# Performance work log

Measured on AMD Instinct MI355X. Metric: run time of the kernel, lower is better.

Reference implementation:

```python
import jax, jax.numpy as jnp
import numpy as np

B, E, H, LEVELS, MAXN = 16, 256, 256, 12, 2
N = 2 ** LEVELS - 1  # 4095 nodes, level-order perfect binary tree
NODE_VOCAB, EDGE_VOCAB = 64, 128

PARAM_SHAPES = {
    'node_emb': (NODE_VOCAB, E), 'edge_emb': (EDGE_VOCAB, E),
    'bu_Wioux': (E, 3 * H), 'bu_bioux': (3 * H,), 'bu_Wfx': (E, H), 'bu_bfx': (H,),
    'bu_Wiouh': (MAXN * H, 3 * H), 'bu_Wfh': (MAXN, MAXN * H, H),
    'bu_eWih': (E, 4 * H), 'bu_eWhh': (H, 4 * H), 'bu_ebih': (4 * H,), 'bu_ebhh': (4 * H,),
    'td_Wioux': (E, 3 * H), 'td_bioux': (3 * H,), 'td_Wfx': (E, H), 'td_bfx': (H,),
    'td_Wiouhc': (MAXN * H, 3 * H), 'td_Wiouhp': (H, 3 * H),
    'td_Wfchild': (MAXN, (MAXN + 1) * H, H), 'td_Wfparent': ((MAXN + 1) * H, H),
    'td_eWih': (E, 4 * H), 'td_eWhh': (H, 4 * H), 'td_ebih': (4 * H,), 'td_ebhh': (4 * H,),
}
FLOAT_NAMES = list(PARAM_SHAPES)

_sig = jax.nn.sigmoid

def _lstm(x, h, c, Wih, Whh, bih, bhh):
    # torch nn.LSTMCell gate order: i, f, g, o
    g = x @ Wih + h @ Whh + bih + bhh
    i, f, gg, o = jnp.split(g, 4, axis=-1)
    c2 = _sig(f) * c + _sig(i) * jnp.tanh(gg)
    return _sig(o) * jnp.tanh(c2), c2

def _forward(p, node_ids, edge_ids):
    x_all = p['node_emb'][node_ids]  # [B,N,E]
    e_all = p['edge_emb'][edge_ids]  # [B,N,E] edge to parent
    bu_h = [None] * LEVELS
    bu_he = [None] * LEVELS
    bu_ce = [None] * LEVELS
    # ---- bottom-up n-ary TreeLSTM, level by level (deepest first) ----
    for l in range(LEVELS - 1, -1, -1):
        M = 2 ** l
        s = M - 1
        x = x_all[:, s:s + M]
        if l == LEVELS - 1:  # leaves: zero-padded children (no fc terms)
            ch_h = jnp.zeros((B, M, MAXN, H), x.dtype)
            ch_c = ch_h
        else:
            ch_h = bu_he[l + 1].reshape(B, M, MAXN, H)
            ch_c = bu_ce[l + 1].reshape(B, M, MAXN, H)
        cat = ch_h.reshape(B, M, MAXN * H)  # child_cat_h
        iou = x @ p['bu_Wioux'] + p['bu_bioux'] + cat @ p['bu_Wiouh']
        i, o, u = jnp.split(iou, 3, axis=-1)
        i, o, u = _sig(i), _sig(o), jnp.tanh(u)
        fx = x @ p['bu_Wfx'] + p['bu_bfx']
        f = _sig(fx[:, :, None, :] + jnp.einsum('bmc,kch->bmkh', cat, p['bu_Wfh']))
        c = i * u + (f * ch_c).sum(axis=2)
        h = o * jnp.tanh(c)
        bu_h[l] = h
        # edge-transition LSTMCell before passing state to parent
        he, ce = _lstm(e_all[:, s:s + M], h, c, p['bu_eWih'], p['bu_eWhh'], p['bu_ebih'], p['bu_ebhh'])
        bu_he[l] = he
        bu_ce[l] = ce
    # ---- top-down n-ary TreeLSTM (root first) ----
    td_h = [None] * LEVELS
    ph = jnp.zeros((B, 1, H), x_all.dtype)
    pc = ph
    for l in range(LEVELS):
        M = 2 ** l
        s = M - 1
        x = x_all[:, s:s + M]
        if l == LEVELS - 1:
            ch_h = jnp.zeros((B, M, MAXN, H), x.dtype)
            ch_c = ch_h
        else:
            ch_h = bu_he[l + 1].reshape(B, M, MAXN, H)
            ch_c = bu_ce[l + 1].reshape(B, M, MAXN, H)
        cat = ch_h.reshape(B, M, MAXN * H)
        iou = x @ p['td_Wioux'] + p['td_bioux'] + cat @ p['td_Wiouhc'] + ph @ p['td_Wiouhp']
        i, o, u = jnp.split(iou, 3, axis=-1)
        i, o, u = _sig(i), _sig(o), jnp.tanh(u)
        fx = x @ p['td_Wfx'] + p['td_bfx']
        pcat = jnp.concatenate([ph, cat], axis=-1)  # [B,M,(MAXN+1)H]
        f_ch = _sig(fx[:, :, None, :] + jnp.einsum('bmc,kch->bmkh', pcat, p['td_Wfchild']))
        f_par = _sig(fx + pcat @ p['td_Wfparent'])
        c = i * u + (f_ch * ch_c).sum(axis=2) + f_par * pc
        h = o * jnp.tanh(c)
        td_h[l] = h
        if l < LEVELS - 1:
            M2 = 2 * M
            s2 = 2 * M - 1
            ph_r = jnp.repeat(h, 2, axis=1)
            pc_r = jnp.repeat(c, 2, axis=1)
            ph, pc = _lstm(e_all[:, s2:s2 + M2], ph_r, pc_r, p['td_eWih'], p['td_eWhh'], p['td_ebih'], p['td_ebhh'])
    return jnp.concatenate([jnp.concatenate(bu_h, 1), jnp.concatenate(td_h, 1)], axis=-1)  # [B,N,2H]


def setup_inputs() -> dict:
    key = jax.random.key(0)
    ks = jax.random.split(key, len(PARAM_SHAPES) + 2)
    inp = {}
    for k, (name, shp) in zip(ks, PARAM_SHAPES.items()):
        inp[name] = jax.random.normal(k, shp, dtype=jnp.float32) * 0.05
    inp['node_ids'] = jax.random.randint(ks[-2], (B, N), 0, NODE_VOCAB)
    inp['edge_ids'] = jax.random.randint(ks[-1], (B, N), 0, EDGE_VOCAB)
    return inp


def reference(node_emb, edge_emb, bu_Wioux, bu_bioux, bu_Wfx, bu_bfx, bu_Wiouh, bu_Wfh,
              bu_eWih, bu_eWhh, bu_ebih, bu_ebhh, td_Wioux, td_bioux, td_Wfx, td_bfx,
              td_Wiouhc, td_Wiouhp, td_Wfchild, td_Wfparent, td_eWih, td_eWhh, td_ebih, td_ebhh,
              node_ids, edge_ids):
    floats = (node_emb, edge_emb, bu_Wioux, bu_bioux, bu_Wfx, bu_bfx, bu_Wiouh, bu_Wfh,
              bu_eWih, bu_eWhh, bu_ebih, bu_ebhh, td_Wioux, td_bioux, td_Wfx, td_bfx,
              td_Wiouhc, td_Wiouhp, td_Wfchild, td_Wfparent, td_eWih, td_eWhh, td_ebih, td_ebhh)
    return _forward(dict(zip(FLOAT_NAMES, floats)), node_ids, edge_ids)
```

## Files before the change

kernel.cpp:

```cpp
#include <hip/hip_runtime.h>
#include <math.h>

#define NB 16
#define NH 256
#define NLV 12
#define NN 4095
#define OUTW 512

typedef unsigned short u16;
typedef unsigned int u32;
typedef __attribute__((ext_vector_type(4))) float f32x4;
typedef __attribute__((ext_vector_type(8))) short bf16x8;

__device__ __forceinline__ float sigf(float x){
  return __fdividef(1.0f, 1.0f + __expf(-x));
}
__device__ __forceinline__ float tanh_fast(float x){
  return 1.0f - __fdividef(2.0f, 1.0f + __expf(2.0f * x));
}

__device__ __forceinline__ u16 f2bf(float x){
  unsigned int u = __float_as_uint(x);
  return (u16)((u + 0x7fffu + ((u >> 16) & 1u)) >> 16);
}
__device__ __forceinline__ float bf2f(u16 h){
  return __uint_as_float(((unsigned int)h) << 16);
}

__device__ __forceinline__ void gload16(const void* g, void* l){
  __builtin_amdgcn_global_load_lds(
      (const __attribute__((address_space(1))) unsigned int*)g,
      (__attribute__((address_space(3))) unsigned int*)l, 16, 0, 0);
}

template<int VAR, int NG>
__global__ __launch_bounds__(256, 2) void fused_gemm(
    int R, int logM, int s,
    const int* __restrict__ ids,
    const u16* __restrict__ emb,
    const u16* __restrict__ hsrc,
    const u16* __restrict__ hsrc2,
    const u16* __restrict__ Wth, int wstride,
    const float* __restrict__ bias,
    const float* __restrict__ cce,
    const float* __restrict__ cprev,
    float* __restrict__ c_out,
    u16* __restrict__ h_out,
    float* __restrict__ out)
{
  constexpr int K0 = 256;
  constexpr int K1 = (VAR == 0) ? 512 : 256;
  constexpr int K2 = (VAR == 2 && NG == 6) ? 512 : 0;
  constexpr int KTOT = K0 + K1 + K2;
  constexpr int NSTEP = KTOT / 64;

  __shared__ u16 As[2][128][64];
  __shared__ u16 Bs[2][NG * 32][64];

  int bx = blockIdx.x;
  if ((gridDim.x & 7) == 0){
    int q = (int)gridDim.x >> 3;
    bx = (bx & 7) * q + (bx >> 3);
  }

  int tid = threadIdx.x, lane = tid & 63, w = tid >> 6;
  int wrow = w >> 1, whh = w & 1;
  int hh0 = blockIdx.y * 32;
  int M = 1 << logM;

  int lrow8 = lane >> 3;
  int gran  = lane & 7;
  int swz = (gran ^ lrow8) * 8;

  u32 off0[4]; u32 off1[4]; u32 off2[4];
  #pragma unroll
  for (int c = 0; c < 4; ++c){
    int gr = bx * 128 + c * 32 + w * 8 + lrow8;
    if (gr > R - 1) gr = R - 1;
    int b = gr >> logM, m = gr & (M - 1);
    int j = s + m;
    off0[c] = (u32)ids[b * NN + j] * 256u + (u32)swz;
    if constexpr (VAR == 0)
      off1[c] = (u32)(b * NN + 2 * j + 1) * (u32)NH + (u32)swz;
    else if constexpr (VAR == 3)
      off1[c] = (u32)(b * (M >> 1) + (m >> 1)) * (u32)NH + (u32)swz;
    else
      off1[c] = (u32)gr * (u32)NH + (u32)swz;
    if constexpr (K2 > 0)
      off2[c] = (u32)(b * NN + 2 * j + 1) * (u32)NH + (u32)swz;
    else
      off2[c] = 0;
  }
  u32 offB = (u32)(hh0 + w * 8 + lrow8) * (u32)wstride + (u32)swz;

  auto stage = [&](int buf, int kt){
    #pragma unroll
    for (int c = 0; c < 4; ++c){
      const u16* ga;
      if (kt < K0)               ga = emb   + off0[c] + kt;
      else if (kt < K0 + K1)     ga = hsrc  + off1[c] + (kt - K0);
      else                       ga = hsrc2 + off2[c] + (kt - K0 - K1);
      gload16(ga, &As[buf][c * 32 + w * 8][0]);
    }
    #pragma unroll
    for (int g = 0; g < NG; ++g)
      gload16(Wth + offB + (u32)(g * 256) * (u32)wstride + kt,
              &Bs[buf][g * 32 + w * 8][0]);
  };

  f32x4 acc[NG][4];
  #pragma unroll
  for (int g = 0; g < NG; ++g)
    #pragma unroll
    for (int i = 0; i < 4; ++i) acc[g][i] = (f32x4)0.0f;

  stage(0, 0);
  __syncthreads();

  #pragma unroll
  for (int st = 0; st < NSTEP; ++st){
    const int cur = st & 1;
    if (st + 1 < NSTEP) stage(cur ^ 1, (st + 1) * 64);

    #pragma unroll
    for (int kc = 0; kc < 2; ++kc){
      int g2 = ((kc * 4 + (lane >> 4)) ^ (lane & 7)) * 8;
      bf16x8 a[4];
      #pragma unroll
      for (int i = 0; i < 4; ++i)
        a[i] = *(const bf16x8*)&As[cur][wrow * 64 + i * 16 + (lane & 15)][g2];
      bf16x8 bf[NG];
      #pragma unroll
      for (int g = 0; g < NG; ++g)
        bf[g] = *(const bf16x8*)&Bs[cur][g * 32 + whh * 16 + (lane & 15)][g2];
      #pragma unroll
      for (int g = 0; g < NG; ++g)
        #pragma unroll
        for (int i = 0; i < 4; ++i)
          acc[g][i] = __builtin_amdgcn_mfma_f32_16x16x32_bf16(a[i], bf[g], acc[g][i], 0, 0, 0);
    }
    __syncthreads();
  }

  int hhL = hh0 + whh * 16 + (lane & 15);
  float bb[NG];
  #pragma unroll
  for (int g = 0; g < NG; ++g) bb[g] = bias[g * 256 + hhL];

  #pragma unroll
  for (int i = 0; i < 4; ++i){
    #pragma unroll
    for (int r = 0; r < 4; ++r){
      int row = bx * 128 + wrow * 64 + i * 16 + ((lane >> 4) << 2) + r;
      if (row >= R) continue;
      int b = row >> logM, m = row & (M - 1);
      int j = s + m;
      if constexpr (VAR == 0){
        float iv = sigf(acc[0][i][r] + bb[0]);
        float ov = sigf(acc[1][i][r] + bb[1]);
        float uv = tanh_fast(acc[2][i][r] + bb[2]);
        float c = iv * uv;
        float f0 = sigf(acc[3][i][r] + bb[3]);
        float f1 = sigf(acc[4 % NG][i][r] + bb[4 % NG]);
        c += f0 * cce[((size_t)(b * NN + 2 * j + 1)) * NH + hhL]
           + f1 * cce[((size_t)(b * NN + 2 * j + 2)) * NH + hhL];
        float h = ov * tanh_fast(c);
        c_out[(size_t)row * NH + hhL] = c;
        h_out[(size_t)row * NH + hhL] = f2bf(h);
        out[((size_t)(b * NN + j)) * OUTW + hhL] = h;
      } else if constexpr (VAR == 1){
        float iv = sigf(acc[0][i][r] + bb[0]);
        float fv = sigf(acc[1][i][r] + bb[1]);
        float gg = tanh_fast(acc[2][i][r] + bb[2]);
        float ov = sigf(acc[3 % NG][i][r] + bb[3 % NG]);
        float c2 = fv * cprev[(size_t)row * NH + hhL] + iv * gg;
        float h2 = ov * tanh_fast(c2);
        size_t di = ((size_t)(b * NN + j)) * NH + hhL;
        h_out[di] = f2bf(h2);
        c_out[di] = c2;
      } else if constexpr (VAR == 2){
        float iv = sigf(acc[0][i][r] + bb[0]);
        float ov = sigf(acc[1][i][r] + bb[1]);
        float uv = tanh_fast(acc[2][i][r] + bb[2]);
        float fp = sigf(acc[3 % NG][i][r] + bb[3 % NG]);
        float c = iv * uv + fp * cprev[(size_t)row * NH + hhL];
        if constexpr (NG == 6){
          float f0 = sigf(acc[4 % NG][i][r] + bb[4 % NG]);
          float f1 = sigf(acc[5 % NG][i][r] + bb[5 % NG]);
          c += f0 * cce[((size_t)(b * NN + 2 * j + 1)) * NH + hhL]
             + f1 * cce[((size_t)(b * NN + 2 * j + 2)) * NH + hhL];
        }
        float h = ov * tanh_fast(c);
        c_out[(size_t)row * NH + hhL] = c;
        h_out[(size_t)row * NH + hhL] = f2bf(h);
        out[((size_t)(b * NN + j)) * OUTW + NH + hhL] = h;
      } else {
        float iv = sigf(acc[0][i][r] + bb[0]);
        float fv = sigf(acc[1][i][r] + bb[1]);
        float gg = tanh_fast(acc[2][i][r] + bb[2]);
        float ov = sigf(acc[3 % NG][i][r] + bb[3 % NG]);
        int par = b * (M >> 1) + (m >> 1);
        float c2 = fv * cprev[(size_t)par * NH + hhL] + iv * gg;
        float h2 = ov * tanh_fast(c2);
        h_out[(size_t)row * NH + hhL] = f2bf(h2);
        c_out[(size_t)row * NH + hhL] = c2;
      }
    }
  }
}

__global__ void build_lut(int nids, int ncols, int stride, int koff,
                          const u16* __restrict__ tab,
                          const u16* __restrict__ Wt, int wstride,
                          const float* __restrict__ bias,
                          float* __restrict__ lut)
{
  int t = blockIdx.x * 256 + threadIdx.x;
  if (t >= nids * ncols) return;
  int id = t / ncols, n = t % ncols;
  const u16* e  = tab + id * 256;
  const u16* wv = Wt + (size_t)n * wstride + koff;
  float z = bias ? bias[n] : 0.0f;
  for (int k = 0; k < 256; k += 8){
    #pragma unroll
    for (int q = 0; q < 8; ++q)
      z += bf2f(e[k + q]) * bf2f(wv[k + q]);
  }
  int hh = n & 255, g = n >> 8;
  lut[((size_t)id * 256 + hh) * stride + g] = z;
}

__global__ void build_leaf(const float* __restrict__ lut64,
                           float* __restrict__ c64, float* __restrict__ h64f,
                           u16* __restrict__ h64b)
{
  int t = blockIdx.x * 256 + threadIdx.x;
  const float* lp = lut64 + (size_t)t * 3;
  float iv = sigf(lp[0]), ov = sigf(lp[1]), uv = tanh_fast(lp[2]);
  float c = iv * uv;
  float h = ov * tanh_fast(c);
  c64[t] = c; h64f[t] = h; h64b[t] = f2bf(h);
}

__global__ void leaf_gather(const int* __restrict__ node_ids,
                            const float* __restrict__ h64f,
                            float* __restrict__ out)
{
  int t = blockIdx.x * 256 + threadIdx.x;
  int gr = t >> 6, q4 = (t & 63) << 2;
  int b = gr >> 11, m = gr & 2047;
  int j = 2047 + m;
  int id = node_ids[b * NN + j];
  float4 hv = *(const float4*)(h64f + id * 256 + q4);
  *(float4*)(out + ((size_t)(b * NN + j)) * OUTW + q4) = hv;
}

__global__ void leaf_edge(const int* __restrict__ node_ids,
                          const int* __restrict__ edge_ids,
                          const float* __restrict__ lutE,
                          const float* __restrict__ lutH,
                          const float* __restrict__ c64,
                          u16* __restrict__ he_b, float* __restrict__ ce_all)
{
  int gr = blockIdx.x;
  int hh = threadIdx.x;
  int b = gr >> 11, m = gr & 2047;
  int j = 2047 + m;
  int nid = node_ids[b * NN + j];
  int eid = edge_ids[b * NN + j];
  float4 ge = *(const float4*)(lutE + ((size_t)eid * 256 + hh) * 4);
  float4 gh = *(const float4*)(lutH + ((size_t)nid * 256 + hh) * 4);
  float iv = sigf(ge.x + gh.x);
  float fv = sigf(ge.y + gh.y);
  float gg = tanh_fast(ge.z + gh.z);
  float ov = sigf(ge.w + gh.w);
  float cp = c64[nid * 256 + hh];
  float c2 = fv * cp + iv * gg;
  float h2 = ov * tanh_fast(c2);
  size_t di = ((size_t)(b * NN + j)) * NH + hh;
  he_b[di] = f2bf(h2);
  ce_all[di] = c2;
}


__global__ void pack_bu_node_t(const float* __restrict__ Wioux, const float* __restrict__ Wiouh,
                               const float* __restrict__ Wfx, const float* __restrict__ Wfh,
                               const float* __restrict__ bioux, const float* __restrict__ bfx,
                               u16* __restrict__ Wth, float* __restrict__ bd)
{
  int tid = blockIdx.x*256 + threadIdx.x;
  if (tid < 768*1280){
    int n = tid / 768, k = tid % 768;
    float v;
    if (n < 768){
      v = (k < 256) ? Wioux[k*768 + n] : Wiouh[(k-256)*768 + n];
    } else {
      int kidx = (n < 1024) ? 0 : 1;
      int nn = n - 768 - kidx*256;
      v = (k < 256) ? Wfx[k*256 + nn] : Wfh[((size_t)kidx*512 + (k-256))*256 + nn];
    }
    Wth[tid] = f2bf(v);
  }
  if (tid < 1280) bd[tid] = (tid < 768) ? bioux[tid] : bfx[(tid-768) & 255];
}

__global__ void pack_edge_t(const float* __restrict__ Wih, const float* __restrict__ Whh,
                            const float* __restrict__ bih, const float* __restrict__ bhh,
                            u16* __restrict__ Wth, float* __restrict__ bd)
{
  int tid = blockIdx.x*256 + threadIdx.x;
  if (tid < 512*1024){
    int n = tid / 512, k = tid % 512;
    float v = (k < 256) ? Wih[k*1024 + n] : Whh[(k-256)*1024 + n];
    Wth[tid] = f2bf(v);
  }
  if (tid < 1024) bd[tid] = bih[tid] + bhh[tid];
}

__global__ void pack_td_node_t(const float* __restrict__ Wioux, const float* __restrict__ Wiouhc,
                               const float* __restrict__ Wiouhp, const float* __restrict__ Wfx,
                               const float* __restrict__ Wfchild, const float* __restrict__ Wfparent,
                               const float* __restrict__ bioux, const float* __restrict__ bfx,
                               u16* __restrict__ Wth, float* __restrict__ bd)
{
  int tid = blockIdx.x*256 + threadIdx.x;
  if (tid < 1024*1536){
    int n = tid / 1024, k = tid % 1024;
    float v;
    if (n < 768){
      v = (k < 256) ? Wioux[k*768 + n]
        : (k < 512) ? Wiouhp[(k-256)*768 + n]
                    : Wiouhc[(k-512)*768 + n];
    } else if (n < 1024){
      int nn = n - 768;
      v = (k < 256) ? Wfx[k*256 + nn] : Wfparent[(size_t)(k-256)*256 + nn];
    } else {
      int kidx = (n < 1280) ? 0 : 1;
      int nn = n - 1024 - kidx*256;
      v = (k < 256) ? Wfx[k*256 + nn]
                    : Wfchild[((size_t)kidx*768 + (k-256))*256 + nn];
    }
    Wth[tid] = f2bf(v);
  }
  if (tid < 1536) bd[tid] = (tid < 768) ? bioux[tid] : bfx[(tid-768) & 255];
}

__global__ void pack_emb(const float* __restrict__ ne, const float* __restrict__ ee,
                         u16* __restrict__ neb, u16* __restrict__ eeb,
                         u16* __restrict__ ph_b, float* __restrict__ pc)
{
  int tid = blockIdx.x*256 + threadIdx.x;
  if (tid < 64*256)  neb[tid] = f2bf(ne[tid]);
  if (tid < 128*256) eeb[tid] = f2bf(ee[tid]);
  if (tid < NB*NH){ ph_b[tid] = 0; pc[tid] = 0.0f; }
}

extern "C" void kernel_launch(void* const* d_in, const int* in_sizes, int n_in,
                              void* d_out, int out_size, void* d_ws, size_t ws_size,
                              hipStream_t stream)
{
  const float* node_emb  = (const float*)d_in[0];
  const float* edge_emb  = (const float*)d_in[1];
  const float* bu_Wioux  = (const float*)d_in[2];
  const float* bu_bioux  = (const float*)d_in[3];
  const float* bu_Wfx    = (const float*)d_in[4];
  const float* bu_bfx    = (const float*)d_in[5];
  const float* bu_Wiouh  = (const float*)d_in[6];
  const float* bu_Wfh    = (const float*)d_in[7];
  const float* bu_eWih   = (const float*)d_in[8];
  const float* bu_eWhh   = (const float*)d_in[9];
  const float* bu_ebih   = (const float*)d_in[10];
  const float* bu_ebhh   = (const float*)d_in[11];
  const float* td_Wioux  = (const float*)d_in[12];
  const float* td_bioux  = (const float*)d_in[13];
  const float* td_Wfx    = (const float*)d_in[14];
  const float* td_bfx    = (const float*)d_in[15];
  const float* td_Wiouhc = (const float*)d_in[16];
  const float* td_Wiouhp = (const float*)d_in[17];
  const float* td_Wfchild= (const float*)d_in[18];
  const float* td_Wfparent=(const float*)d_in[19];
  const float* td_eWih   = (const float*)d_in[20];
  const float* td_eWhh   = (const float*)d_in[21];
  const float* td_ebih   = (const float*)d_in[22];
  const float* td_ebhh   = (const float*)d_in[23];
  const int* node_ids    = (const int*)d_in[24];
  const int* edge_ids    = (const int*)d_in[25];
  float* out = (float*)d_out;

  float* fw = (float*)d_ws;
  size_t fo = 0;
  float* bbun = fw + fo; fo += 1280;
  float* bbue = fw + fo; fo += 1024;
  float* btdn = fw + fo; fo += 1536;
  float* btde = fw + fo; fo += 1024;
  float* lut64 = fw + fo; fo += (size_t)64*256*3;
  float* c64  = fw + fo; fo += (size_t)64*256;
  float* h64f = fw + fo; fo += (size_t)64*256;
  float* lutE = fw + fo; fo += (size_t)128*256*4;
  float* lutH = fw + fo; fo += (size_t)64*256*4;
  float* ce_all = fw + fo; fo += (size_t)NB*NN*NH;
  float* c_lvl  = fw + fo; fo += (size_t)NB*2048*NH;
  float* pc     = fw + fo; fo += (size_t)NB*2048*NH;

  u16* uw = (u16*)(fw + fo);
  size_t uo = 0;
  u16* Wbunh = uw + uo; uo += (size_t)768*1280;
  u16* Wbueh = uw + uo; uo += (size_t)512*1024;
  u16* Wtdnh = uw + uo; uo += (size_t)1024*1536;
  u16* Wtdeh = uw + uo; uo += (size_t)512*1024;
  u16* neb = uw + uo; uo += (size_t)64*256;
  u16* eeb = uw + uo; uo += (size_t)128*256;
  u16* h64b = uw + uo; uo += (size_t)64*256;
  u16* he_b = uw + uo; uo += (size_t)NB*NN*NH;
  u16* hl_b = uw + uo; uo += (size_t)NB*2048*NH;
  u16* ph_b = uw + uo; uo += (size_t)NB*2048*NH;

  pack_bu_node_t<<<(768*1280+255)/256, 256, 0, stream>>>(bu_Wioux, bu_Wiouh, bu_Wfx, bu_Wfh,
      bu_bioux, bu_bfx, Wbunh, bbun);
  pack_edge_t<<<(512*1024+255)/256, 256, 0, stream>>>(bu_eWih, bu_eWhh, bu_ebih, bu_ebhh,
      Wbueh, bbue);
  pack_td_node_t<<<(1024*1536+255)/256, 256, 0, stream>>>(td_Wioux, td_Wiouhc, td_Wiouhp, td_Wfx,
      td_Wfchild, td_Wfparent, td_bioux, td_bfx, Wtdnh, btdn);
  pack_edge_t<<<(512*1024+255)/256, 256, 0, stream>>>(td_eWih, td_eWhh, td_ebih, td_ebhh,
      Wtdeh, btde);
  pack_emb<<<(128*256+255)/256, 256, 0, stream>>>(node_emb, edge_emb, neb, eeb, ph_b, pc);

  build_lut<<<(64*768+255)/256, 256, 0, stream>>>(64, 768, 3, 0, neb, Wbunh, 768, bbun, lut64);
  build_leaf<<<64, 256, 0, stream>>>(lut64, c64, h64f, h64b);
  build_lut<<<(128*1024+255)/256, 256, 0, stream>>>(128, 1024, 4, 0,   eeb,  Wbueh, 512, bbue,  lutE);
  build_lut<<<(64*1024+255)/256, 256, 0, stream>>>(64,  1024, 4, 256, h64b, Wbueh, 512, nullptr, lutH);

  {
    int R = NB * 2048;
    leaf_gather<<<(R * 64) / 256, 256, 0, stream>>>(node_ids, h64f, out);
    leaf_edge<<<R, 256, 0, stream>>>(node_ids, edge_ids, lutE, lutH, c64, he_b, ce_all);
  }
  for (int l = NLV-2; l >= 0; --l){
    int M = 1<<l, s = M-1, R = NB*M;
    dim3 grid((R + 127) / 128, NH / 32);
    fused_gemm<0,5><<<grid, 256, 0, stream>>>(R, l, s, node_ids,
        neb, he_b, neb, Wbunh, 768, bbun,
        ce_all, nullptr, c_lvl, hl_b, out);
    if (l > 0){
      fused_gemm<1,4><<<grid, 256, 0, stream>>>(R, l, s, edge_ids,
          eeb, hl_b, neb, Wbueh, 512, bbue,
          nullptr, c_lvl, ce_all, he_b, nullptr);
    }
  }

  for (int l = 0; l < NLV; ++l){
    int M = 1<<l, s = M-1, R = NB*M;
    bool leaf = (l == NLV-1);
    dim3 grid((R + 127) / 128, NH / 32);
    if (!leaf){
      fused_gemm<2,6><<<grid, 256, 0, stream>>>(R, l, s, node_ids,
          neb, ph_b, he_b, Wtdnh, 1024, btdn,
          ce_all, pc, c_lvl, hl_b, out);
      int M2 = 2*M, s2 = 2*M-1, R2 = NB*M2;
      dim3 grid2((R2 + 127) / 128, NH / 32);
      fused_gemm<3,4><<<grid2, 256, 0, stream>>>(R2, l+1, s2, edge_ids,
          eeb, hl_b, neb, Wtdeh, 512, btde,
          nullptr, c_lvl, pc, ph_b, nullptr);
    } else {
      fused_gemm<2,4><<<grid, 256, 0, stream>>>(R, l, s, node_ids,
          neb, ph_b, neb, Wtdnh, 1024, btdn,
          nullptr, pc, c_lvl, hl_b, out);
    }
  }
}
```

Measured before the change: 1.138 ms.

## Replace embedding GEMM K-slice with per-id precomputed gate lookup tables

Because node and edge embeddings come from small vocabularies, the x@W plus bias contribution is precomputed per vocab id into LUTs (stride 8 floats per hidden unit). Every fused GEMM then drops its first 256-wide K slice and adds the LUT value in the epilogue instead. This removes a quarter to a third of the MFMA and staging work per level, at the cost of extra LUT build kernels and scattered per-row LUT loads in the epilogue. The leaf edge kernel is adapted to the new stride-8 LUT layout.

```diff
diff --git a/kernel.cpp b/kernel.cpp
--- a/kernel.cpp
+++ b/kernel.cpp
@@ -37,21 +37,19 @@
 __global__ __launch_bounds__(256, 2) void fused_gemm(
     int R, int logM, int s,
     const int* __restrict__ ids,
-    const u16* __restrict__ emb,
+    const float* __restrict__ lutG,
     const u16* __restrict__ hsrc,
     const u16* __restrict__ hsrc2,
     const u16* __restrict__ Wth, int wstride,
-    const float* __restrict__ bias,
     const float* __restrict__ cce,
     const float* __restrict__ cprev,
     float* __restrict__ c_out,
     u16* __restrict__ h_out,
     float* __restrict__ out)
 {
-  constexpr int K0 = 256;
   constexpr int K1 = (VAR == 0) ? 512 : 256;
   constexpr int K2 = (VAR == 2 && NG == 6) ? 512 : 0;
-  constexpr int KTOT = K0 + K1 + K2;
+  constexpr int KTOT = K1 + K2;
   constexpr int NSTEP = KTOT / 64;
 
   __shared__ u16 As[2][128][64];
@@ -72,14 +70,13 @@
   int gran  = lane & 7;
   int swz = (gran ^ lrow8) * 8;
 
-  u32 off0[4]; u32 off1[4]; u32 off2[4];
+  u32 off1[4]; u32 off2[4];
   #pragma unroll
   for (int c = 0; c < 4; ++c){
     int gr = bx * 128 + c * 32 + w * 8 + lrow8;
     if (gr > R - 1) gr = R - 1;
     int b = gr >> logM, m = gr & (M - 1);
     int j = s + m;
-    off0[c] = (u32)ids[b * NN + j] * 256u + (u32)swz;
     if constexpr (VAR == 0)
       off1[c] = (u32)(b * NN + 2 * j + 1) * (u32)NH + (u32)swz;
     else if constexpr (VAR == 3)
@@ -91,15 +88,14 @@
     else
       off2[c] = 0;
   }
-  u32 offB = (u32)(hh0 + w * 8 + lrow8) * (u32)wstride + (u32)swz;
+  u32 offB = (u32)(hh0 + w * 8 + lrow8) * (u32)wstride + (u32)swz + 256u;
 
   auto stage = [&](int buf, int kt){
     #pragma unroll
     for (int c = 0; c < 4; ++c){
       const u16* ga;
-      if (kt < K0)               ga = emb   + off0[c] + kt;
-      else if (kt < K0 + K1)     ga = hsrc  + off1[c] + (kt - K0);
-      else                       ga = hsrc2 + off2[c] + (kt - K0 - K1);
+      if (K2 > 0 && kt >= K1) ga = hsrc2 + off2[c] + (kt - K1);
+      else                    ga = hsrc  + off1[c] + kt;
       gload16(ga, &As[buf][c * 32 + w * 8][0]);
     }
     #pragma unroll
@@ -143,9 +139,6 @@
   }
 
   int hhL = hh0 + whh * 16 + (lane & 15);
-  float bb[NG];
-  #pragma unroll
-  for (int g = 0; g < NG; ++g) bb[g] = bias[g * 256 + hhL];
 
   #pragma unroll
   for (int i = 0; i < 4; ++i){
@@ -155,13 +148,14 @@
       if (row >= R) continue;
       int b = row >> logM, m = row & (M - 1);
       int j = s + m;
+      const float* lp = lutG + ((size_t)ids[b * NN + j] * 256 + hhL) * 8;
       if constexpr (VAR == 0){
-        float iv = sigf(acc[0][i][r] + bb[0]);
-        float ov = sigf(acc[1][i][r] + bb[1]);
-        float uv = tanh_fast(acc[2][i][r] + bb[2]);
+        float iv = sigf(acc[0][i][r] + lp[0]);
+        float ov = sigf(acc[1][i][r] + lp[1]);
+        float uv = tanh_fast(acc[2][i][r] + lp[2]);
         float c = iv * uv;
-        float f0 = sigf(acc[3][i][r] + bb[3]);
-        float f1 = sigf(acc[4 % NG][i][r] + bb[4 % NG]);
+        float f0 = sigf(acc[3][i][r] + lp[3]);
+        float f1 = sigf(acc[4 % NG][i][r] + lp[4]);
         c += f0 * cce[((size_t)(b * NN + 2 * j + 1)) * NH + hhL]
            + f1 * cce[((size_t)(b * NN + 2 * j + 2)) * NH + hhL];
         float h = ov * tanh_fast(c);
@@ -169,24 +163,24 @@
         h_out[(size_t)row * NH + hhL] = f2bf(h);
         out[((size_t)(b * NN + j)) * OUTW + hhL] = h;
       } else if constexpr (VAR == 1){
-        float iv = sigf(acc[0][i][r] + bb[0]);
-        float fv = sigf(acc[1][i][r] + bb[1]);
-        float gg = tanh_fast(acc[2][i][r] + bb[2]);
-        float ov = sigf(acc[3 % NG][i][r] + bb[3 % NG]);
+        float iv = sigf(acc[0][i][r] + lp[0]);
+        float fv = sigf(acc[1][i][r] + lp[1]);
+        float gg = tanh_fast(acc[2][i][r] + lp[2]);
+        float ov = sigf(acc[3 % NG][i][r] + lp[3]);
         float c2 = fv * cprev[(size_t)row * NH + hhL] + iv * gg;
         float h2 = ov * tanh_fast(c2);
         size_t di = ((size_t)(b * NN + j)) * NH + hhL;
         h_out[di] = f2bf(h2);
         c_out[di] = c2;
       } else if constexpr (VAR == 2){
-        float iv = sigf(acc[0][i][r] + bb[0]);
-        float ov = sigf(acc[1][i][r] + bb[1]);
-        float uv = tanh_fast(acc[2][i][r] + bb[2]);
-        float fp = sigf(acc[3 % NG][i][r] + bb[3 % NG]);
+        float iv = sigf(acc[0][i][r] + lp[0]);
+        float ov = sigf(acc[1][i][r] + lp[1]);
+        float uv = tanh_fast(acc[2][i][r] + lp[2]);
+        float fp = sigf(acc[3 % NG][i][r] + lp[3]);
         float c = iv * uv + fp * cprev[(size_t)row * NH + hhL];
         if constexpr (NG == 6){
-          float f0 = sigf(acc[4 % NG][i][r] + bb[4 % NG]);
-          float f1 = sigf(acc[5 % NG][i][r] + bb[5 % NG]);
+          float f0 = sigf(acc[4 % NG][i][r] + lp[4]);
+          float f1 = sigf(acc[5 % NG][i][r] + lp[5]);
           c += f0 * cce[((size_t)(b * NN + 2 * j + 1)) * NH + hhL]
              + f1 * cce[((size_t)(b * NN + 2 * j + 2)) * NH + hhL];
         }
@@ -195,10 +189,10 @@
         h_out[(size_t)row * NH + hhL] = f2bf(h);
         out[((size_t)(b * NN + j)) * OUTW + NH + hhL] = h;
       } else {
-        float iv = sigf(acc[0][i][r] + bb[0]);
-        float fv = sigf(acc[1][i][r] + bb[1]);
-        float gg = tanh_fast(acc[2][i][r] + bb[2]);
-        float ov = sigf(acc[3 % NG][i][r] + bb[3 % NG]);
+        float iv = sigf(acc[0][i][r] + lp[0]);
+        float fv = sigf(acc[1][i][r] + lp[1]);
+        float gg = tanh_fast(acc[2][i][r] + lp[2]);
+        float ov = sigf(acc[3 % NG][i][r] + lp[3]);
         int par = b * (M >> 1) + (m >> 1);
         float c2 = fv * cprev[(size_t)par * NH + hhL] + iv * gg;
         float h2 = ov * tanh_fast(c2);
@@ -268,12 +262,12 @@
   int j = 2047 + m;
   int nid = node_ids[b * NN + j];
   int eid = edge_ids[b * NN + j];
-  float4 ge = *(const float4*)(lutE + ((size_t)eid * 256 + hh) * 4);
-  float4 gh = *(const float4*)(lutH + ((size_t)nid * 256 + hh) * 4);
-  float iv = sigf(ge.x + gh.x);
-  float fv = sigf(ge.y + gh.y);
-  float gg = tanh_fast(ge.z + gh.z);
-  float ov = sigf(ge.w + gh.w);
+  const float* pe = lutE + ((size_t)eid * 256 + hh) * 8;
+  const float* ph = lutH + ((size_t)nid * 256 + hh) * 8;
+  float iv = sigf(pe[0] + ph[0]);
+  float fv = sigf(pe[1] + ph[1]);
+  float gg = tanh_fast(pe[2] + ph[2]);
+  float ov = sigf(pe[3] + ph[3]);
   float cp = c64[nid * 256 + hh];
   float c2 = fv * cp + iv * gg;
   float h2 = ov * tanh_fast(c2);
@@ -396,8 +390,11 @@
   float* lut64 = fw + fo; fo += (size_t)64*256*3;
   float* c64  = fw + fo; fo += (size_t)64*256;
   float* h64f = fw + fo; fo += (size_t)64*256;
-  float* lutE = fw + fo; fo += (size_t)128*256*4;
-  float* lutH = fw + fo; fo += (size_t)64*256*4;
+  float* lutBUN = fw + fo; fo += (size_t)64*256*8;
+  float* lutTDN = fw + fo; fo += (size_t)64*256*8;
+  float* lutBUE = fw + fo; fo += (size_t)128*256*8;
+  float* lutTDE = fw + fo; fo += (size_t)128*256*8;
+  float* lutH   = fw + fo; fo += (size_t)64*256*8;
   float* ce_all = fw + fo; fo += (size_t)NB*NN*NH;
   float* c_lvl  = fw + fo; fo += (size_t)NB*2048*NH;
   float* pc     = fw + fo; fo += (size_t)NB*2048*NH;
@@ -427,23 +424,26 @@
 
   build_lut<<<(64*768+255)/256, 256, 0, stream>>>(64, 768, 3, 0, neb, Wbunh, 768, bbun, lut64);
   build_leaf<<<64, 256, 0, stream>>>(lut64, c64, h64f, h64b);
-  build_lut<<<(128*1024+255)/256, 256, 0, stream>>>(128, 1024, 4, 0,   eeb,  Wbueh, 512, bbue,  lutE);
-  build_lut<<<(64*1024+255)/256, 256, 0, stream>>>(64,  1024, 4, 256, h64b, Wbueh, 512, nullptr, lutH);
+  build_lut<<<(64*1280+255)/256, 256, 0, stream>>>(64, 1280, 8, 0, neb, Wbunh, 768, bbun, lutBUN);
+  build_lut<<<(64*1536+255)/256, 256, 0, stream>>>(64, 1536, 8, 0, neb, Wtdnh, 1024, btdn, lutTDN);
+  build_lut<<<(128*1024+255)/256, 256, 0, stream>>>(128, 1024, 8, 0, eeb, Wbueh, 512, bbue, lutBUE);
+  build_lut<<<(128*1024+255)/256, 256, 0, stream>>>(128, 1024, 8, 0, eeb, Wtdeh, 512, btde, lutTDE);
+  build_lut<<<(64*1024+255)/256, 256, 0, stream>>>(64, 1024, 8, 256, h64b, Wbueh, 512, nullptr, lutH);
 
   {
     int R = NB * 2048;
     leaf_gather<<<(R * 64) / 256, 256, 0, stream>>>(node_ids, h64f, out);
-    leaf_edge<<<R, 256, 0, stream>>>(node_ids, edge_ids, lutE, lutH, c64, he_b, ce_all);
+    leaf_edge<<<R, 256, 0, stream>>>(node_ids, edge_ids, lutBUE, lutH, c64, he_b, ce_all);
   }
   for (int l = NLV-2; l >= 0; --l){
     int M = 1<<l, s = M-1, R = NB*M;
     dim3 grid((R + 127) / 128, NH / 32);
     fused_gemm<0,5><<<grid, 256, 0, stream>>>(R, l, s, node_ids,
-        neb, he_b, neb, Wbunh, 768, bbun,
+        lutBUN, he_b, nullptr, Wbunh, 768,
         ce_all, nullptr, c_lvl, hl_b, out);
     if (l > 0){
       fused_gemm<1,4><<<grid, 256, 0, stream>>>(R, l, s, edge_ids,
-          eeb, hl_b, neb, Wbueh, 512, bbue,
+          lutBUE, hl_b, nullptr, Wbueh, 512,
           nullptr, c_lvl, ce_all, he_b, nullptr);
     }
   }
@@ -454,16 +454,16 @@
     dim3 grid((R + 127) / 128, NH / 32);
     if (!leaf){
       fused_gemm<2,6><<<grid, 256, 0, stream>>>(R, l, s, node_ids,
-          neb, ph_b, he_b, Wtdnh, 1024, btdn,
+          lutTDN, ph_b, he_b, Wtdnh, 1024,
           ce_all, pc, c_lvl, hl_b, out);
       int M2 = 2*M, s2 = 2*M-1, R2 = NB*M2;
       dim3 grid2((R2 + 127) / 128, NH / 32);
       fused_gemm<3,4><<<grid2, 256, 0, stream>>>(R2, l+1, s2, edge_ids,
-          eeb, hl_b, neb, Wtdeh, 512, btde,
+          lutTDE, hl_b, nullptr, Wtdeh, 512,
           nullptr, c_lvl, pc, ph_b, nullptr);
     } else {
       fused_gemm<2,4><<<grid, 256, 0, stream>>>(R, l, s, node_ids,
-          neb, ph_b, neb, Wtdnh, 1024, btdn,
+          lutTDN, ph_b, nullptr, Wtdnh, 1024,
           nullptr, pc, c_lvl, hl_b, out);
     }
   }
```

Result: no change. 1.151 ms (+1.2%).
